# Kernel optimization log

Hardware: AMD Instinct MI355X
Metric: run time of the kernel (lower is better)

## Reference

```python
import jax, jax.numpy as jnp
import numpy as np

B, S, H, D = 4, 8192, 8, 64  # batch, seq, heads, head_dim
M = 64                        # num random features
EPS = 1e-6


def setup_inputs() -> dict:
    key = jax.random.key(0)
    k1, k2, k3, k4 = jax.random.split(key, 4)
    qs = jax.random.normal(k1, (B, S, H, D), dtype=jnp.float32)
    ks = jax.random.normal(k2, (B, S, H, D), dtype=jnp.float32)
    vs = jax.random.normal(k3, (B, S, H, D), dtype=jnp.float32)
    proj = jax.random.normal(k4, (M, D), dtype=jnp.float32)
    return {"qs": qs, "ks": ks, "vs": vs, "proj": proj}


def _phi(x, proj):
    # stable positive softmax kernel: exp(x @ proj^T - ||x||^2/2) / sqrt(m)
    m = proj.shape[0]
    x_proj = jnp.einsum('...d,md->...m', x, proj)
    h = jnp.sum(jnp.square(x), axis=-1, keepdims=True) * 0.5
    return jnp.exp(x_proj - h) / jnp.sqrt(jnp.asarray(m, x.dtype))


def reference(qs, ks, vs, proj):
    Bq, Q, Hh, Dqk = qs.shape
    K = ks.shape[1]
    Dv = vs.shape[-1]
    # (B, S, H, D) -> (B*H, S, D)
    q = qs.transpose(0, 2, 1, 3).reshape(-1, Q, Dqk)
    k = ks.transpose(0, 2, 1, 3).reshape(-1, K, Dqk)
    v = vs.transpose(0, 2, 1, 3).reshape(-1, K, Dv)
    normalizer = 1.0 / jnp.power(jnp.asarray(Dqk, q.dtype), 0.25)
    q_prime = _phi(q * normalizer, proj)  # (B*H, Q, M)
    k_prime = _phi(k * normalizer, proj)  # (B*H, K, M)
    # fast_attend: linear-time attention
    c = jnp.concatenate([v, jnp.ones((*v.shape[:-1], 1), v.dtype)], axis=-1)  # (B*H, K, Dv+1)
    buf1 = jnp.einsum('bkm,bkc->bmc', k_prime, c)   # (B*H, M, Dv+1)
    buf2 = jnp.einsum('bqm,bmc->bqc', q_prime, buf1)  # (B*H, Q, Dv+1)
    num, den = buf2[..., :-1], buf2[..., -1]
    den = jnp.where(den < EPS, EPS, den)
    ctx = num / den[..., None]
    return ctx.reshape(Bq, Hh, Q, Dv).transpose(0, 2, 1, 3)
```

## Files before the change

kernel.cpp:

```cpp
#include <hip/hip_runtime.h>
#include <hip/hip_bf16.h>

#define S_ 8192
#define H_ 8
#define D_ 64
#define M_ 64
#define BH_ 32
#define CPK_ 80
#define NCHK 32
#define NCHQ 16
#define TILE 64
#define QTILES (S_ / NCHQ / TILE)

typedef short bf16x8 __attribute__((ext_vector_type(8)));
typedef float f32x4 __attribute__((ext_vector_type(4)));

constexpr float XS_ = 0.35355339059327373f * 1.4426950408889634f;
constexpr float HS_ = 0.34657359027997264f;
constexpr float EPS_ = 1e-6f;

__device__ __forceinline__ unsigned short f2bf(float f) {
    unsigned int u = __float_as_uint(f);
    u += 0x7FFFu + ((u >> 16) & 1u);
    return (unsigned short)(u >> 16);
}
__device__ __forceinline__ unsigned int pkbf(float lo, float hi) {
    __hip_bfloat162 t = __float22bfloat162_rn(float2{lo, hi});
    return *reinterpret_cast<unsigned int*>(&t);
}
__device__ __forceinline__ float fexp2(float x) { return __builtin_amdgcn_exp2f(x); }

#define MFMA(a, b, c) __builtin_amdgcn_mfma_f32_16x16x32_bf16((a), (b), (c), 0, 0, 0)
#define SWZ(byteoff, row) ((byteoff) ^ (((row) & 7) << 4))

#define GLDS(src, dst) __builtin_amdgcn_global_load_lds( \
    (const __attribute__((address_space(1))) void*)(src), \
    (__attribute__((address_space(3))) void*)(dst), 16, 0, 0)

__global__ void __launch_bounds__(128)
fa_k(const float* __restrict__ ks, const float* __restrict__ vs,
     const float* __restrict__ proj, float* __restrict__ partial)
{
    __shared__ __align__(16) char pool[2][4][8192];

    const int chunk = blockIdx.x;
    const int bh    = blockIdx.y;
    const int b = bh >> 3, h = bh & 7;
    const int tid = threadIdx.x, wid = tid >> 6, lane = tid & 63;
    const int l15 = lane & 15, g = lane >> 4;

    const size_t rs = (size_t)H_ * D_;
    const float* kb = ks + ((size_t)b * S_ * H_ + h) * D_;
    const float* vb = vs + ((size_t)b * S_ * H_ + h) * D_;
    const int rbase = chunk * 256 + wid * 128;

    bf16x8 pf[4][2];
#pragma unroll
    for (int mt = 0; mt < 4; ++mt)
#pragma unroll
        for (int kk = 0; kk < 2; ++kk) {
            const float* p = proj + (mt * 16 + l15) * D_ + kk * 32 + g * 8;
            float4 a = *(const float4*)p, c = *(const float4*)(p + 4);
            union { bf16x8 v; unsigned int u[4]; } F;
            F.u[0] = pkbf(a.x, a.y); F.u[1] = pkbf(a.z, a.w);
            F.u[2] = pkbf(c.x, c.y); F.u[3] = pkbf(c.z, c.w);
            pf[mt][kk] = F.v;
        }

    bf16x8 onef = {0, 0, 0, 0, 0, 0, 0, 0};
    if (l15 == 0) {
#pragma unroll
        for (int j = 0; j < 8; ++j) onef[j] = (short)0x3F80;
    }

    f32x4 acc[4][5];
#pragma unroll
    for (int mt = 0; mt < 4; ++mt)
#pragma unroll
        for (int ci = 0; ci < 5; ++ci) acc[mt][ci] = (f32x4){0.f, 0.f, 0.f, 0.f};

    auto stage = [&](int t) {
        char* kd = pool[wid][t & 3];
        char* vd = kd + 4096;
        const float* krow = kb + (size_t)(rbase + t * 16 + l15) * rs;
        const float* vrow = vb + (size_t)(rbase + t * 16 + l15) * rs;
#pragma unroll
        for (int i = 0; i < 4; ++i) {
            int c0 = (i >> 1) * 32 + (i & 1) * 4 + 8 * g;
            GLDS(krow + c0, kd + i * 1024);
            GLDS(vrow + c0, vd + i * 1024);
        }
    };

    f32x4 paE[4], paO[4];
    float hrE[4], hrO[4];

    auto consumeP = [&](int t, f32x4* pa, float* hr) {
        const char* kd = pool[wid][t & 3];
        f32x4 r0 = *(const f32x4*)(kd + lane * 16);
        f32x4 r1 = *(const f32x4*)(kd + 1024 + lane * 16);
        f32x4 r2 = *(const f32x4*)(kd + 2048 + lane * 16);
        f32x4 r3 = *(const f32x4*)(kd + 3072 + lane * 16);
        float kx[16];
#pragma unroll
        for (int j = 0; j < 4; ++j) {
            kx[j]      = r0[j] * XS_;
            kx[4 + j]  = r1[j] * XS_;
            kx[8 + j]  = r2[j] * XS_;
            kx[12 + j] = r3[j] * XS_;
        }
        float sq = 0.f;
#pragma unroll
        for (int j = 0; j < 16; ++j) sq += kx[j] * kx[j];
        sq += __shfl_xor(sq, 16);
        sq += __shfl_xor(sq, 32);
        float hrow = sq * HS_ + 3.0f;

        union { bf16x8 v; unsigned int u[4]; } A0, A1;
#pragma unroll
        for (int i = 0; i < 4; ++i) {
            A0.u[i] = pkbf(kx[2 * i], kx[2 * i + 1]);
            A1.u[i] = pkbf(kx[8 + 2 * i], kx[9 + 2 * i]);
        }
#pragma unroll
        for (int mt = 0; mt < 4; ++mt) {
            pa[mt] = (f32x4){0.f, 0.f, 0.f, 0.f};
            pa[mt] = MFMA(A0.v, pf[mt][0], pa[mt]);
            pa[mt] = MFMA(A1.v, pf[mt][1], pa[mt]);
        }
#pragma unroll
        for (int r = 0; r < 4; ++r) hr[r] = __shfl(hrow, 4 * g + r);
    };

    auto EV = [&](int t) {
        const char* vE = pool[wid][t & 3] + 4096;
        const char* vO = pool[wid][(t + 1) & 3] + 4096;
        bf16x8 eA[4];
#pragma unroll
        for (int mt = 0; mt < 4; ++mt) {
            union { bf16x8 v; unsigned int u[4]; } E;
            E.u[0] = pkbf(fexp2(paE[mt][0] - hrE[0]), fexp2(paE[mt][1] - hrE[1]));
            E.u[1] = pkbf(fexp2(paE[mt][2] - hrE[2]), fexp2(paE[mt][3] - hrE[3]));
            E.u[2] = pkbf(fexp2(paO[mt][0] - hrO[0]), fexp2(paO[mt][1] - hrO[1]));
            E.u[3] = pkbf(fexp2(paO[mt][2] - hrO[2]), fexp2(paO[mt][3] - hrO[3]));
            eA[mt] = E.v;
        }
#pragma unroll
        for (int ct = 0; ct < 4; ++ct) {
            int c = ct * 16 + l15;
            int ic = ((c >> 5) << 1) | ((c >> 2) & 1);
            int boff = ic * 1024 + ((c & 31) >> 3) * 256 + (c & 3) * 4 + 64 * g;
            float e0 = *(const float*)(vE + boff);
            float e1 = *(const float*)(vE + boff + 16);
            float e2 = *(const float*)(vE + boff + 32);
            float e3 = *(const float*)(vE + boff + 48);
            float o0 = *(const float*)(vO + boff);
            float o1 = *(const float*)(vO + boff + 16);
            float o2 = *(const float*)(vO + boff + 32);
            float o3 = *(const float*)(vO + boff + 48);
            union { bf16x8 v; unsigned int u[4]; } B;
            B.u[0] = pkbf(e0, e1); B.u[1] = pkbf(e2, e3);
            B.u[2] = pkbf(o0, o1); B.u[3] = pkbf(o2, o3);
#pragma unroll
            for (int mt = 0; mt < 4; ++mt)
                acc[mt][ct] = MFMA(eA[mt], B.v, acc[mt][ct]);
        }
#pragma unroll
        for (int mt = 0; mt < 4; ++mt)
            acc[mt][4] = MFMA(eA[mt], onef, acc[mt][4]);
    };

    stage(0); stage(1); stage(2); stage(3);

#define PAIR(T, W1, W2, DOSTAGE)                                   \
    asm volatile("s_waitcnt vmcnt(" #W1 ")" ::: "memory");         \
    __builtin_amdgcn_sched_barrier(0);                             \
    consumeP(T, paE, hrE);                                         \
    asm volatile("s_waitcnt vmcnt(" #W2 ")" ::: "memory");         \
    __builtin_amdgcn_sched_barrier(0);                             \
    consumeP(T + 1, paO, hrO);                                     \
    EV(T);                                                         \
    if (DOSTAGE) { stage(T + 4); stage(T + 5); }

    PAIR(0, 24, 16, 1)
    PAIR(2, 24, 16, 1)
    PAIR(4, 24, 16, 0)
    PAIR(6, 8, 0, 0)
#undef PAIR

    __syncthreads();
    float* red = (float*)pool;
    for (int i = tid; i < M_ * CPK_; i += 128) red[i] = 0.f;
    __syncthreads();
    for (int w = 0; w < 2; ++w) {
        if (wid == w) {
#pragma unroll
            for (int mt = 0; mt < 4; ++mt)
#pragma unroll
                for (int ct = 0; ct < 5; ++ct)
#pragma unroll
                    for (int r = 0; r < 4; ++r)
                        red[(mt * 16 + 4 * g + r) * CPK_ + ct * 16 + l15] +=
                            acc[mt][ct][r];
        }
        __syncthreads();
    }
    float* dst = partial + ((size_t)bh * NCHK + chunk) * (M_ * CPK_);
    for (int i = tid; i < M_ * CPK_; i += 128) dst[i] = red[i];
}

__global__ void __launch_bounds__(256)
fa_r(const float* __restrict__ partial, float* __restrict__ buf1, int nch)
{
    int e = blockIdx.x * 256 + threadIdx.x;
    if (e >= BH_ * M_ * CPK_) return;
    int bh = e / (M_ * CPK_);
    int r  = e - bh * (M_ * CPK_);
    const float* src = partial + (size_t)bh * nch * (M_ * CPK_) + r;
    float s0 = 0.f, s1 = 0.f, s2 = 0.f, s3 = 0.f;
    int ch = 0;
    for (; ch + 4 <= nch; ch += 4) {
        s0 += src[(size_t)(ch + 0) * (M_ * CPK_)];
        s1 += src[(size_t)(ch + 1) * (M_ * CPK_)];
        s2 += src[(size_t)(ch + 2) * (M_ * CPK_)];
        s3 += src[(size_t)(ch + 3) * (M_ * CPK_)];
    }
    for (; ch < nch; ++ch) s0 += src[(size_t)ch * (M_ * CPK_)];
    buf1[e] = (s0 + s1) + (s2 + s3);
}

__global__ void __launch_bounds__(256)
fa_q(const float* __restrict__ qs, const float* __restrict__ proj,
     const float* __restrict__ buf1, float* __restrict__ out)
{
    const int chunk = blockIdx.x;
    const int bh    = blockIdx.y;
    const int b = bh >> 3, h = bh & 7;
    const int tid = threadIdx.x, wid = tid >> 6, lane = tid & 63;
    const int l15 = lane & 15, g = lane >> 4;

    __shared__ __align__(16) char eLb[2][TILE * M_ * 2];
    __shared__ __align__(16) char b1tb[CPK_ * M_ * 2];

    const int rows = S_ / NCHQ;
    const int s0 = chunk * rows;
    const size_t rs = (size_t)H_ * D_;
    const float* qb = qs + ((size_t)b * S_ * H_ + h) * D_;

    const float* b1 = buf1 + (size_t)bh * (M_ * CPK_);
    for (int i = tid; i < M_ * CPK_; i += 256) {
        int m = i / CPK_, c = i - m * CPK_;
        *(unsigned short*)(b1tb + SWZ(c * 128 + 2 * m, c)) = f2bf(b1[i]);
    }

    bf16x8 pf[4][2];
#pragma unroll
    for (int mt = 0; mt < 4; ++mt)
#pragma unroll
        for (int kk = 0; kk < 2; ++kk) {
            const float* p = proj + (mt * 16 + l15) * D_ + kk * 32 + g * 8;
            float4 a = *(const float4*)p, c = *(const float4*)(p + 4);
            union { bf16x8 v; unsigned int u[4]; } F;
            F.u[0] = pkbf(a.x, a.y); F.u[1] = pkbf(a.z, a.w);
            F.u[2] = pkbf(c.x, c.y); F.u[3] = pkbf(c.z, c.w);
            pf[mt][kk] = F.v;
        }
    __syncthreads();

    bf16x8 af3[5][2];
#pragma unroll
    for (int ci = 0; ci < 5; ++ci)
#pragma unroll
        for (int kk = 0; kk < 2; ++kk) {
            int c = ci * 16 + l15;
            af3[ci][kk] = *(const bf16x8*)(b1tb + SWZ(c * 128 + 16 * g + 64 * kk, c));
        }

    auto loadQ = [&](int t, float4* qp) {
        int sb = s0 + t * TILE;
        const float* qrow = qb + (size_t)(sb + wid * 16 + l15) * rs;
        qp[0] = *(const float4*)(qrow + g * 8);
        qp[1] = *(const float4*)(qrow + g * 8 + 4);
        qp[2] = *(const float4*)(qrow + 32 + g * 8);
        qp[3] = *(const float4*)(qrow + 32 + g * 8 + 4);
    };

    auto body = [&](int t, int p, const float4* qc, float4* qn) {
        if (t + 1 < QTILES) loadQ(t + 1, qn);

        float kx[16];
#pragma unroll
        for (int i = 0; i < 4; ++i) {
            kx[4 * i + 0] = qc[i].x * XS_; kx[4 * i + 1] = qc[i].y * XS_;
            kx[4 * i + 2] = qc[i].z * XS_; kx[4 * i + 3] = qc[i].w * XS_;
        }
        float sq = 0.f;
#pragma unroll
        for (int j = 0; j < 16; ++j) sq += kx[j] * kx[j];
        sq += __shfl_xor(sq, 16);
        sq += __shfl_xor(sq, 32);
        float hrow = sq * HS_ + 3.0f;

        union { bf16x8 v; unsigned int u[4]; } A0, A1;
#pragma unroll
        for (int i = 0; i < 4; ++i) {
            A0.u[i] = pkbf(kx[2 * i], kx[2 * i + 1]);
            A1.u[i] = pkbf(kx[8 + 2 * i], kx[9 + 2 * i]);
        }

        f32x4 pa[4];
#pragma unroll
        for (int mt = 0; mt < 4; ++mt) {
            pa[mt] = (f32x4){0.f, 0.f, 0.f, 0.f};
            pa[mt] = MFMA(A0.v, pf[mt][0], pa[mt]);
            pa[mt] = MFMA(A1.v, pf[mt][1], pa[mt]);
        }

        float hr[4];
#pragma unroll
        for (int r = 0; r < 4; ++r) hr[r] = __shfl(hrow, 4 * g + r);

        char* elp = eLb[p];
#pragma unroll
        for (int mt = 0; mt < 4; ++mt) {
            int m = mt * 16 + l15;
            float e0 = fexp2(pa[mt][0] - hr[0]);
            float e1 = fexp2(pa[mt][1] - hr[1]);
            float e2 = fexp2(pa[mt][2] - hr[2]);
            float e3 = fexp2(pa[mt][3] - hr[3]);
            unsigned int p01 = pkbf(e0, e1), p23 = pkbf(e2, e3);
            int q0 = wid * 16 + 4 * g;
            *(unsigned short*)(elp + SWZ((q0 + 0) * 128 + 2 * m, q0 + 0)) =
                (unsigned short)p01;
            *(unsigned short*)(elp + SWZ((q0 + 1) * 128 + 2 * m, q0 + 1)) =
                (unsigned short)(p01 >> 16);
            *(unsigned short*)(elp + SWZ((q0 + 2) * 128 + 2 * m, q0 + 2)) =
                (unsigned short)p23;
            *(unsigned short*)(elp + SWZ((q0 + 3) * 128 + 2 * m, q0 + 3)) =
                (unsigned short)(p23 >> 16);
        }
        __syncthreads();

        bf16x8 b3[2];
        {
            int qrow = wid * 16 + l15;
            b3[0] = *(const bf16x8*)(elp + SWZ(qrow * 128 + 16 * g, qrow));
            b3[1] = *(const bf16x8*)(elp + SWZ(qrow * 128 + 16 * g + 64, qrow));
        }
        f32x4 dt[5];
#pragma unroll
        for (int ci = 0; ci < 5; ++ci) {
            dt[ci] = (f32x4){0.f, 0.f, 0.f, 0.f};
            dt[ci] = MFMA(af3[ci][0], b3[0], dt[ci]);
            dt[ci] = MFMA(af3[ci][1], b3[1], dt[ci]);
        }

        float den = __shfl(dt[4][0], l15);
        float rd = 1.0f / fmaxf(den, EPS_);

        int sg = s0 + t * TILE + wid * 16 + l15;
        size_t base = (((size_t)b * S_ + sg) * H_ + h) * D_;
#pragma unroll
        for (int ci = 0; ci < 4; ++ci) {
            f32x4 o;
#pragma unroll
            for (int r = 0; r < 4; ++r) o[r] = dt[ci][r] * rd;
            *(f32x4*)(out + base + ci * 16 + 4 * g) = o;
        }
    };

    float4 qa[4], qb2[4];
    loadQ(0, qa);
    for (int t = 0; t < QTILES; t += 2) {
        body(t, 0, qa, qb2);
        body(t + 1, 1, qb2, qa);
    }
}

extern "C" void kernel_launch(void* const* d_in, const int* in_sizes, int n_in,
                              void* d_out, int out_size, void* d_ws, size_t ws_size,
                              hipStream_t stream)
{
    const float* qs   = (const float*)d_in[0];
    const float* ks   = (const float*)d_in[1];
    const float* vs   = (const float*)d_in[2];
    const float* proj = (const float*)d_in[3];
    float* out = (float*)d_out;

    float* partial = (float*)d_ws;
    float* buf1 = partial + (size_t)BH_ * NCHK * (M_ * CPK_);

    fa_k<<<dim3(NCHK, BH_), 128, 0, stream>>>(ks, vs, proj, partial);
    int nred = (BH_ * M_ * CPK_ + 255) / 256;
    fa_r<<<dim3(nred), 256, 0, stream>>>(partial, buf1, NCHK);
    fa_q<<<dim3(NCHQ, BH_), 256, 0, stream>>>(qs, proj, buf1, out);
}
```

Measured before the change: 81.70 us.

## Use single-wave K blocks with double buffering and direct partial stores

Restructures the K/V reduction kernel so each block is one 64-thread wave that handles 128 rows, with two LDS buffers instead of a four-deep per-wave pool. The launch grid doubles to 64 chunks per head, with a fallback to 32 chunks and two segments when the workspace is too small. V operands are packed into registers as each tile is consumed, and accumulators are written straight to the partial buffer. This removes the shared-memory cross-wave reduction and its barriers. In exchange the prefetch depth is shallower and the fa_r reduction has more partials to sum.

```diff
diff --git a/kernel.cpp b/kernel.cpp
--- a/kernel.cpp
+++ b/kernel.cpp
@@ -7,7 +7,7 @@
 #define M_ 64
 #define BH_ 32
 #define CPK_ 80
-#define NCHK 32
+#define MC_ (M_ * CPK_)
 #define NCHQ 16
 #define TILE 64
 #define QTILES (S_ / NCHQ / TILE)
@@ -37,22 +37,23 @@
     (const __attribute__((address_space(1))) void*)(src), \
     (__attribute__((address_space(3))) void*)(dst), 16, 0, 0)
 
-__global__ void __launch_bounds__(128)
+__global__ void __launch_bounds__(64, 2)
 fa_k(const float* __restrict__ ks, const float* __restrict__ vs,
-     const float* __restrict__ proj, float* __restrict__ partial)
+     const float* __restrict__ proj, float* __restrict__ partial,
+     int nch, int segs)
 {
-    __shared__ __align__(16) char pool[2][4][8192];
+    __shared__ __align__(16) char bufA[8192];
+    __shared__ __align__(16) char bufB[8192];
 
     const int chunk = blockIdx.x;
     const int bh    = blockIdx.y;
     const int b = bh >> 3, h = bh & 7;
-    const int tid = threadIdx.x, wid = tid >> 6, lane = tid & 63;
+    const int lane = threadIdx.x & 63;
     const int l15 = lane & 15, g = lane >> 4;
 
     const size_t rs = (size_t)H_ * D_;
     const float* kb = ks + ((size_t)b * S_ * H_ + h) * D_;
     const float* vb = vs + ((size_t)b * S_ * H_ + h) * D_;
-    const int rbase = chunk * 256 + wid * 128;
 
     bf16x8 pf[4][2];
 #pragma unroll
@@ -79,153 +80,146 @@
 #pragma unroll
         for (int ci = 0; ci < 5; ++ci) acc[mt][ci] = (f32x4){0.f, 0.f, 0.f, 0.f};
 
-    auto stage = [&](int t) {
-        char* kd = pool[wid][t & 3];
-        char* vd = kd + 4096;
-        const float* krow = kb + (size_t)(rbase + t * 16 + l15) * rs;
-        const float* vrow = vb + (size_t)(rbase + t * 16 + l15) * rs;
-#pragma unroll
-        for (int i = 0; i < 4; ++i) {
-            int c0 = (i >> 1) * 32 + (i & 1) * 4 + 8 * g;
-            GLDS(krow + c0, kd + i * 1024);
-            GLDS(vrow + c0, vd + i * 1024);
-        }
-    };
-
     f32x4 paE[4], paO[4];
     float hrE[4], hrO[4];
-
-    auto consumeP = [&](int t, f32x4* pa, float* hr) {
-        const char* kd = pool[wid][t & 3];
-        f32x4 r0 = *(const f32x4*)(kd + lane * 16);
-        f32x4 r1 = *(const f32x4*)(kd + 1024 + lane * 16);
-        f32x4 r2 = *(const f32x4*)(kd + 2048 + lane * 16);
-        f32x4 r3 = *(const f32x4*)(kd + 3072 + lane * 16);
-        float kx[16];
-#pragma unroll
-        for (int j = 0; j < 4; ++j) {
-            kx[j]      = r0[j] * XS_;
-            kx[4 + j]  = r1[j] * XS_;
-            kx[8 + j]  = r2[j] * XS_;
-            kx[12 + j] = r3[j] * XS_;
-        }
-        float sq = 0.f;
-#pragma unroll
-        for (int j = 0; j < 16; ++j) sq += kx[j] * kx[j];
-        sq += __shfl_xor(sq, 16);
-        sq += __shfl_xor(sq, 32);
-        float hrow = sq * HS_ + 3.0f;
-
-        union { bf16x8 v; unsigned int u[4]; } A0, A1;
-#pragma unroll
-        for (int i = 0; i < 4; ++i) {
-            A0.u[i] = pkbf(kx[2 * i], kx[2 * i + 1]);
-            A1.u[i] = pkbf(kx[8 + 2 * i], kx[9 + 2 * i]);
-        }
-#pragma unroll
-        for (int mt = 0; mt < 4; ++mt) {
-            pa[mt] = (f32x4){0.f, 0.f, 0.f, 0.f};
-            pa[mt] = MFMA(A0.v, pf[mt][0], pa[mt]);
-            pa[mt] = MFMA(A1.v, pf[mt][1], pa[mt]);
-        }
-#pragma unroll
-        for (int r = 0; r < 4; ++r) hr[r] = __shfl(hrow, 4 * g + r);
-    };
-
-    auto EV = [&](int t) {
-        const char* vE = pool[wid][t & 3] + 4096;
-        const char* vO = pool[wid][(t + 1) & 3] + 4096;
-        bf16x8 eA[4];
-#pragma unroll
-        for (int mt = 0; mt < 4; ++mt) {
-            union { bf16x8 v; unsigned int u[4]; } E;
-            E.u[0] = pkbf(fexp2(paE[mt][0] - hrE[0]), fexp2(paE[mt][1] - hrE[1]));
-            E.u[1] = pkbf(fexp2(paE[mt][2] - hrE[2]), fexp2(paE[mt][3] - hrE[3]));
-            E.u[2] = pkbf(fexp2(paO[mt][0] - hrO[0]), fexp2(paO[mt][1] - hrO[1]));
-            E.u[3] = pkbf(fexp2(paO[mt][2] - hrO[2]), fexp2(paO[mt][3] - hrO[3]));
-            eA[mt] = E.v;
-        }
-#pragma unroll
-        for (int ct = 0; ct < 4; ++ct) {
-            int c = ct * 16 + l15;
-            int ic = ((c >> 5) << 1) | ((c >> 2) & 1);
-            int boff = ic * 1024 + ((c & 31) >> 3) * 256 + (c & 3) * 4 + 64 * g;
-            float e0 = *(const float*)(vE + boff);
-            float e1 = *(const float*)(vE + boff + 16);
-            float e2 = *(const float*)(vE + boff + 32);
-            float e3 = *(const float*)(vE + boff + 48);
-            float o0 = *(const float*)(vO + boff);
-            float o1 = *(const float*)(vO + boff + 16);
-            float o2 = *(const float*)(vO + boff + 32);
-            float o3 = *(const float*)(vO + boff + 48);
-            union { bf16x8 v; unsigned int u[4]; } B;
-            B.u[0] = pkbf(e0, e1); B.u[1] = pkbf(e2, e3);
-            B.u[2] = pkbf(o0, o1); B.u[3] = pkbf(o2, o3);
-#pragma unroll
-            for (int mt = 0; mt < 4; ++mt)
-                acc[mt][ct] = MFMA(eA[mt], B.v, acc[mt][ct]);
-        }
-#pragma unroll
-        for (int mt = 0; mt < 4; ++mt)
-            acc[mt][4] = MFMA(eA[mt], onef, acc[mt][4]);
-    };
-
-    stage(0); stage(1); stage(2); stage(3);
-
-#define PAIR(T, W1, W2, DOSTAGE)                                   \
-    asm volatile("s_waitcnt vmcnt(" #W1 ")" ::: "memory");         \
-    __builtin_amdgcn_sched_barrier(0);                             \
-    consumeP(T, paE, hrE);                                         \
-    asm volatile("s_waitcnt vmcnt(" #W2 ")" ::: "memory");         \
-    __builtin_amdgcn_sched_barrier(0);                             \
-    consumeP(T + 1, paO, hrO);                                     \
-    EV(T);                                                         \
-    if (DOSTAGE) { stage(T + 4); stage(T + 5); }
-
-    PAIR(0, 24, 16, 1)
-    PAIR(2, 24, 16, 1)
-    PAIR(4, 24, 16, 0)
-    PAIR(6, 8, 0, 0)
-#undef PAIR
-
-    __syncthreads();
-    float* red = (float*)pool;
-    for (int i = tid; i < M_ * CPK_; i += 128) red[i] = 0.f;
-    __syncthreads();
-    for (int w = 0; w < 2; ++w) {
-        if (wid == w) {
-#pragma unroll
-            for (int mt = 0; mt < 4; ++mt)
-#pragma unroll
-                for (int ct = 0; ct < 5; ++ct)
-#pragma unroll
-                    for (int r = 0; r < 4; ++r)
-                        red[(mt * 16 + 4 * g + r) * CPK_ + ct * 16 + l15] +=
-                            acc[mt][ct][r];
-        }
-        __syncthreads();
-    }
-    float* dst = partial + ((size_t)bh * NCHK + chunk) * (M_ * CPK_);
-    for (int i = tid; i < M_ * CPK_; i += 128) dst[i] = red[i];
+    unsigned int vbu[4][4];
+
+#define STAGE(T, BUF) do {                                                  \
+    const float* krow_ = kb + (size_t)(rbase + (T) * 16 + l15) * rs;        \
+    const float* vrow_ = vb + (size_t)(rbase + (T) * 16 + l15) * rs;        \
+    _Pragma("unroll")                                                       \
+    for (int i_ = 0; i_ < 4; ++i_) {                                        \
+        int c0_ = (i_ >> 1) * 32 + (i_ & 1) * 4 + 8 * g;                    \
+        GLDS(krow_ + c0_, (BUF) + i_ * 1024);                               \
+        GLDS(vrow_ + c0_, (BUF) + 4096 + i_ * 1024);                        \
+    } } while (0)
+
+#define CONSUME(BUF, PA, HR) do {                                           \
+    f32x4 r0_ = *(const f32x4*)((BUF) + lane * 16);                         \
+    f32x4 r1_ = *(const f32x4*)((BUF) + 1024 + lane * 16);                  \
+    f32x4 r2_ = *(const f32x4*)((BUF) + 2048 + lane * 16);                  \
+    f32x4 r3_ = *(const f32x4*)((BUF) + 3072 + lane * 16);                  \
+    float kx_[16];                                                          \
+    _Pragma("unroll")                                                       \
+    for (int j_ = 0; j_ < 4; ++j_) {                                        \
+        kx_[j_]      = r0_[j_] * XS_;  kx_[4 + j_]  = r1_[j_] * XS_;        \
+        kx_[8 + j_]  = r2_[j_] * XS_;  kx_[12 + j_] = r3_[j_] * XS_;        \
+    }                                                                       \
+    float sq_ = 0.f;                                                        \
+    _Pragma("unroll")                                                       \
+    for (int j_ = 0; j_ < 16; ++j_) sq_ += kx_[j_] * kx_[j_];               \
+    sq_ += __shfl_xor(sq_, 16);                                             \
+    sq_ += __shfl_xor(sq_, 32);                                             \
+    float hrow_ = sq_ * HS_ + 3.0f;                                         \
+    union { bf16x8 v; unsigned int u[4]; } A0_, A1_;                        \
+    _Pragma("unroll")                                                       \
+    for (int i_ = 0; i_ < 4; ++i_) {                                        \
+        A0_.u[i_] = pkbf(kx_[2 * i_], kx_[2 * i_ + 1]);                     \
+        A1_.u[i_] = pkbf(kx_[8 + 2 * i_], kx_[9 + 2 * i_]);                 \
+    }                                                                       \
+    _Pragma("unroll")                                                       \
+    for (int mt_ = 0; mt_ < 4; ++mt_) {                                     \
+        PA[mt_] = (f32x4){0.f, 0.f, 0.f, 0.f};                              \
+        PA[mt_] = MFMA(A0_.v, pf[mt_][0], PA[mt_]);                         \
+        PA[mt_] = MFMA(A1_.v, pf[mt_][1], PA[mt_]);                         \
+    }                                                                       \
+    _Pragma("unroll")                                                       \
+    for (int r_ = 0; r_ < 4; ++r_) HR[r_] = __shfl(hrow_, 4 * g + r_);      \
+    } while (0)
+
+#define VHALF(BUF, I0, I1) do {                                             \
+    const char* vd_ = (BUF) + 4096;                                         \
+    _Pragma("unroll")                                                       \
+    for (int ct_ = 0; ct_ < 4; ++ct_) {                                     \
+        int c_ = ct_ * 16 + l15;                                            \
+        int ic_ = ((c_ >> 5) << 1) | ((c_ >> 2) & 1);                       \
+        int boff_ = ic_ * 1024 + ((c_ & 31) >> 3) * 256 + (c_ & 3) * 4      \
+                  + 64 * g;                                                 \
+        float e0_ = *(const float*)(vd_ + boff_);                           \
+        float e1_ = *(const float*)(vd_ + boff_ + 16);                      \
+        float e2_ = *(const float*)(vd_ + boff_ + 32);                      \
+        float e3_ = *(const float*)(vd_ + boff_ + 48);                      \
+        vbu[ct_][I0] = pkbf(e0_, e1_);                                      \
+        vbu[ct_][I1] = pkbf(e2_, e3_);                                      \
+    } } while (0)
+
+#define EVREG() do {                                                        \
+    _Pragma("unroll")                                                       \
+    for (int mt_ = 0; mt_ < 4; ++mt_) {                                     \
+        union { bf16x8 v; unsigned int u[4]; } E_;                          \
+        E_.u[0] = pkbf(fexp2(paE[mt_][0] - hrE[0]),                         \
+                       fexp2(paE[mt_][1] - hrE[1]));                        \
+        E_.u[1] = pkbf(fexp2(paE[mt_][2] - hrE[2]),                         \
+                       fexp2(paE[mt_][3] - hrE[3]));                        \
+        E_.u[2] = pkbf(fexp2(paO[mt_][0] - hrO[0]),                         \
+                       fexp2(paO[mt_][1] - hrO[1]));                        \
+        E_.u[3] = pkbf(fexp2(paO[mt_][2] - hrO[2]),                         \
+                       fexp2(paO[mt_][3] - hrO[3]));                        \
+        _Pragma("unroll")                                                   \
+        for (int ct_ = 0; ct_ < 4; ++ct_) {                                 \
+            union { bf16x8 v; unsigned int u[4]; } B_;                      \
+            B_.u[0] = vbu[ct_][0]; B_.u[1] = vbu[ct_][1];                   \
+            B_.u[2] = vbu[ct_][2]; B_.u[3] = vbu[ct_][3];                   \
+            acc[mt_][ct_] = MFMA(E_.v, B_.v, acc[mt_][ct_]);                \
+        }                                                                   \
+        acc[mt_][4] = MFMA(E_.v, onef, acc[mt_][4]);                        \
+    } } while (0)
+
+#define WAIT8 do { asm volatile("s_waitcnt vmcnt(8)" ::: "memory");         \
+                   __builtin_amdgcn_sched_barrier(0); } while (0)
+#define WAIT0 do { asm volatile("s_waitcnt vmcnt(0)" ::: "memory");         \
+                   __builtin_amdgcn_sched_barrier(0); } while (0)
+
+    for (int seg = 0; seg < segs; ++seg) {
+        const int rbase = (chunk * segs + seg) * 128;
+
+        STAGE(0, bufA); STAGE(1, bufB);
+
+        WAIT8; CONSUME(bufA, paE, hrE); VHALF(bufA, 0, 1); STAGE(2, bufA);
+        WAIT8; CONSUME(bufB, paO, hrO); VHALF(bufB, 2, 3); STAGE(3, bufB);
+        EVREG();
+
+        WAIT8; CONSUME(bufA, paE, hrE); VHALF(bufA, 0, 1); STAGE(4, bufA);
+        WAIT8; CONSUME(bufB, paO, hrO); VHALF(bufB, 2, 3); STAGE(5, bufB);
+        EVREG();
+
+        WAIT8; CONSUME(bufA, paE, hrE); VHALF(bufA, 0, 1); STAGE(6, bufA);
+        WAIT8; CONSUME(bufB, paO, hrO); VHALF(bufB, 2, 3); STAGE(7, bufB);
+        EVREG();
+
+        WAIT8; CONSUME(bufA, paE, hrE); VHALF(bufA, 0, 1);
+        WAIT0; CONSUME(bufB, paO, hrO); VHALF(bufB, 2, 3);
+        EVREG();
+    }
+
+    float* dst = partial + ((size_t)bh * nch + chunk) * MC_;
+#pragma unroll
+    for (int mt = 0; mt < 4; ++mt)
+#pragma unroll
+        for (int ct = 0; ct < 5; ++ct)
+#pragma unroll
+            for (int r = 0; r < 4; ++r)
+                dst[(mt * 16 + 4 * g + r) * CPK_ + ct * 16 + l15] =
+                    acc[mt][ct][r];
 }
 
 __global__ void __launch_bounds__(256)
 fa_r(const float* __restrict__ partial, float* __restrict__ buf1, int nch)
 {
     int e = blockIdx.x * 256 + threadIdx.x;
-    if (e >= BH_ * M_ * CPK_) return;
-    int bh = e / (M_ * CPK_);
-    int r  = e - bh * (M_ * CPK_);
-    const float* src = partial + (size_t)bh * nch * (M_ * CPK_) + r;
+    if (e >= BH_ * MC_) return;
+    int bh = e / MC_;
+    int r  = e - bh * MC_;
+    const float* src = partial + (size_t)bh * nch * MC_ + r;
     float s0 = 0.f, s1 = 0.f, s2 = 0.f, s3 = 0.f;
     int ch = 0;
     for (; ch + 4 <= nch; ch += 4) {
-        s0 += src[(size_t)(ch + 0) * (M_ * CPK_)];
-        s1 += src[(size_t)(ch + 1) * (M_ * CPK_)];
-        s2 += src[(size_t)(ch + 2) * (M_ * CPK_)];
-        s3 += src[(size_t)(ch + 3) * (M_ * CPK_)];
-    }
-    for (; ch < nch; ++ch) s0 += src[(size_t)ch * (M_ * CPK_)];
+        s0 += src[(size_t)(ch + 0) * MC_];
+        s1 += src[(size_t)(ch + 1) * MC_];
+        s2 += src[(size_t)(ch + 2) * MC_];
+        s3 += src[(size_t)(ch + 3) * MC_];
+    }
+    for (; ch < nch; ++ch) s0 += src[(size_t)ch * MC_];
     buf1[e] = (s0 + s1) + (s2 + s3);
 }
 
@@ -247,8 +241,8 @@
     const size_t rs = (size_t)H_ * D_;
     const float* qb = qs + ((size_t)b * S_ * H_ + h) * D_;
 
-    const float* b1 = buf1 + (size_t)bh * (M_ * CPK_);
-    for (int i = tid; i < M_ * CPK_; i += 256) {
+    const float* b1 = buf1 + (size_t)bh * MC_;
+    for (int i = tid; i < MC_; i += 256) {
         int m = i / CPK_, c = i - m * CPK_;
         *(unsigned short*)(b1tb + SWZ(c * 128 + 2 * m, c)) = f2bf(b1[i]);
     }
@@ -387,11 +381,16 @@
     const float* proj = (const float*)d_in[3];
     float* out = (float*)d_out;
 
+    int nch = 64, segs = 1;
+    if ((size_t)BH_ * (size_t)(nch + 1) * MC_ * sizeof(float) > ws_size) {
+        nch = 32; segs = 2;
+    }
+
     float* partial = (float*)d_ws;
-    float* buf1 = partial + (size_t)BH_ * NCHK * (M_ * CPK_);
-
-    fa_k<<<dim3(NCHK, BH_), 128, 0, stream>>>(ks, vs, proj, partial);
-    int nred = (BH_ * M_ * CPK_ + 255) / 256;
-    fa_r<<<dim3(nred), 256, 0, stream>>>(partial, buf1, NCHK);
+    float* buf1 = partial + (size_t)BH_ * nch * MC_;
+
+    fa_k<<<dim3(nch, BH_), 64, 0, stream>>>(ks, vs, proj, partial, nch, segs);
+    int nred = (BH_ * MC_ + 255) / 256;
+    fa_r<<<dim3(nred), 256, 0, stream>>>(partial, buf1, nch);
     fa_q<<<dim3(NCHQ, BH_), 256, 0, stream>>>(qs, proj, buf1, out);
 }
```

Result: slower. 90.40 us (+10.7%).
